# Performance work log

Measured on AMD Instinct MI355X. Metric: run time of the kernel, lower is better.

## Reference

```python
import jax, jax.numpy as jnp
import numpy as np

B, M, T, N = 128, 256, 512, 512

def setup_inputs() -> dict:
    key = jax.random.key(0)
    ks = jax.random.split(key, 6)
    return {
        "hidden_state": jax.random.normal(ks[0], (B, M), jnp.float32),
        "cell_state": jax.random.normal(ks[1], (B, M), jnp.float32),
        "X": jax.random.normal(ks[2], (B, T, N), jnp.float32),
        "We1": jax.random.normal(ks[3], (2 * M, T), jnp.float32) * 0.05,
        "be1": jnp.zeros((T,), jnp.float32),
        "We2": jax.random.normal(ks[4], (T, T), jnp.float32) * 0.05,
        "be2": jnp.zeros((T,), jnp.float32),
        "v": jax.random.normal(ks[5], (T, 1), jnp.float32) * 0.05,
        "bv": jnp.zeros((1,), jnp.float32),
    }

def reference(hidden_state, cell_state, X, We1, be1, We2, be2, v, bv):
    # concat hidden + cell: [B, 2m]; Dense(T) then broadcast over n (K.repeat)
    hc = jnp.concatenate([hidden_state, cell_state], axis=-1)
    hs = (hc @ We1 + be1)[:, None, :]                 # [B, 1, T] (broadcast over n)
    # Permute X -> [B, n, T], Dense(T): contract over T
    ux = jnp.einsum('btn,tk->bnk', X, We2) + be2      # [B, n, T]
    # add + tanh + Dense(1) fused chain
    e = jnp.tanh(hs + ux) @ v + bv                    # [B, n, 1]
    # Permute -> [B, 1, n], softmax over last axis (n)
    attn = jax.nn.softmax(jnp.swapaxes(e, 1, 2), axis=-1)  # [B, 1, n]
    return attn
```

## Files before the change

### kernel.cpp

```cpp
#include <hip/hip_runtime.h>
#include <hip/hip_bf16.h>


typedef _Float16 half8 __attribute__((ext_vector_type(8)));
typedef _Float16 half4 __attribute__((ext_vector_type(4)));
typedef float floatx4 __attribute__((ext_vector_type(4)));

#define GLOAD_LDS16(gp, lp) __builtin_amdgcn_global_load_lds(                  \
    (const __attribute__((address_space(1))) void*)(const void*)(gp),          \
    (__attribute__((address_space(3))) void*)(void*)(lp), 16, 0, 0)

__device__ __forceinline__ float fast_tanh(float x) {
    float cx = fminf(15.0f, fmaxf(-15.0f, x));
    float e = __expf(2.0f * cx);
    return (e - 1.0f) * __fdividef(1.0f, e + 1.0f);
}

__global__ __launch_bounds__(256) void k_prep_a(const float* __restrict__ We2,
                                                _Float16* __restrict__ Af) {
    __shared__ float w2[32][512];
    const int ts = blockIdx.x;
    for (int idx = threadIdx.x; idx < 32 * 512; idx += 256) {
        int tl = idx >> 9, k = idx & 511;
        w2[tl][k] = We2[(ts * 32 + tl) * 512 + k];
    }
    __syncthreads();
    for (int item = threadIdx.x; item < 32 * 64; item += 256) {
        int c = item >> 6, l = item & 63;
        int k  = c * 16 + (l & 15);
        int tl = (l >> 4) * 8;
        half8 h;
#pragma unroll
        for (int j = 0; j < 8; ++j) h[j] = (_Float16)w2[tl + j][k];
        *(half8*)&Af[(((size_t)ts * 32 + c) * 64 + l) * 8] = h;
    }
}

__global__ __launch_bounds__(256) void k_hs(const float* __restrict__ hidden,
                                            const float* __restrict__ cell,
                                            const float* __restrict__ We1,
                                            const float* __restrict__ be1,
                                            const float* __restrict__ be2,
                                            float* __restrict__ g) {
    __shared__ __align__(16) float hcl[8][512];
    __shared__ float red[4][8][64];
    const int b0 = (blockIdx.x >> 3) << 3;
    const int k0 = (blockIdx.x & 7) << 6;
    for (int idx = threadIdx.x; idx < 8 * 512; idx += 256) {
        int bi = idx >> 9, j = idx & 511;
        hcl[bi][j] = (j < 256) ? hidden[(b0 + bi) * 256 + j]
                               : cell[(b0 + bi) * 256 + j - 256];
    }
    __syncthreads();
    const int kl = threadIdx.x & 63;
    const int jc = threadIdx.x >> 6;
    const int k  = k0 + kl;
    float acc[8] = {};
    for (int j = jc * 128; j < jc * 128 + 128; j += 4) {
        float w0 = We1[(j + 0) * 512 + k];
        float w1 = We1[(j + 1) * 512 + k];
        float w2 = We1[(j + 2) * 512 + k];
        float w3 = We1[(j + 3) * 512 + k];
#pragma unroll
        for (int bi = 0; bi < 8; ++bi) {
            float4 h = *(const float4*)&hcl[bi][j];
            acc[bi] += h.x * w0 + h.y * w1 + h.z * w2 + h.w * w3;
        }
    }
#pragma unroll
    for (int bi = 0; bi < 8; ++bi) red[jc][bi][kl] = acc[bi];
    __syncthreads();
    for (int idx = threadIdx.x; idx < 512; idx += 256) {
        int bi = idx >> 6, kk = idx & 63;
        float s = red[0][bi][kk] + red[1][bi][kk] + red[2][bi][kk] + red[3][bi][kk];
        int kg = k0 + kk;
        g[(b0 + bi) * 512 + kg] = s + be1[kg] + be2[kg];
    }
}

__global__ __launch_bounds__(512, 4) void k_main(const float* __restrict__ X,
                                                 const _Float16* __restrict__ Af,
                                                 const float* __restrict__ g,
                                                 const float* __restrict__ vvec,
                                                 float* __restrict__ E) {
    __shared__ __align__(16) _Float16 Ab[2][16384];
    __shared__ __align__(16) _Float16 Xb[2][2048];
    const int b    = blockIdx.x >> 3;
    const int n0   = (blockIdx.x & 7) << 6;
    const int tid  = threadIdx.x;
    const int lane = tid & 63;
    const int wv   = tid >> 6;
    const int l16  = lane & 15;
    const int lhi  = lane >> 4;

    const float* Xg = X + (size_t)b * (512 * 512) + n0;
    const int xn = lane;
    const int xslot = ((xn >> 4) * 64 + (wv >> 1) * 16 + (xn & 15)) * 8 + (wv & 1) * 4;
    const _Float16* AgW = Af + (size_t)wv * 2048 + (size_t)lane * 8;

    float xrA[4], xrB[4];

#pragma unroll
    for (int i = 0; i < 4; ++i)
        GLOAD_LDS16(AgW + i * 512, &Ab[0][wv * 2048 + i * 512 + lane * 8]);
#pragma unroll
    for (int j = 0; j < 4; ++j)
        xrA[j] = Xg[(size_t)(wv * 4 + j) * 512 + xn];
#pragma unroll
    for (int j = 0; j < 4; ++j)
        xrB[j] = Xg[(size_t)(32 + wv * 4 + j) * 512 + xn];
    {
        half4 h;
#pragma unroll
        for (int j = 0; j < 4; ++j) h[j] = (_Float16)xrA[j];
        *(half4*)&Xb[0][xslot] = h;
    }
    asm volatile("s_waitcnt vmcnt(4) lgkmcnt(0)" ::: "memory");
    __builtin_amdgcn_sched_barrier(0);
    __builtin_amdgcn_s_barrier();
    __builtin_amdgcn_sched_barrier(0);

    floatx4 acc[4][4];
#pragma unroll
    for (int a = 0; a < 4; ++a)
#pragma unroll
        for (int c = 0; c < 4; ++c) acc[a][c] = (floatx4){0.f, 0.f, 0.f, 0.f};

#pragma unroll
    for (int ts = 0; ts < 16; ++ts) {
        const int cur = ts & 1;
        const int nxt = cur ^ 1;
        if (ts < 15) {
#pragma unroll
            for (int i = 0; i < 4; ++i)
                GLOAD_LDS16(AgW + (size_t)(ts + 1) * 16384 + i * 512,
                            &Ab[nxt][wv * 2048 + i * 512 + lane * 8]);
        }
        if (ts < 14) {
            if ((ts & 1) == 0) {
#pragma unroll
                for (int j = 0; j < 4; ++j)
                    xrA[j] = Xg[(size_t)((ts + 2) * 32 + wv * 4 + j) * 512 + xn];
            } else {
#pragma unroll
                for (int j = 0; j < 4; ++j)
                    xrB[j] = Xg[(size_t)((ts + 2) * 32 + wv * 4 + j) * 512 + xn];
            }
        }
        if (ts < 15) {
            half4 h;
            if ((ts & 1) == 0) {
#pragma unroll
                for (int j = 0; j < 4; ++j) h[j] = (_Float16)xrB[j];
            } else {
#pragma unroll
                for (int j = 0; j < 4; ++j) h[j] = (_Float16)xrA[j];
            }
            *(half4*)&Xb[nxt][xslot] = h;
        }
        {
            half8 af0 = *(const half8*)&Ab[cur][(wv * 4 + 0) * 512 + lane * 8];
            half8 af1 = *(const half8*)&Ab[cur][(wv * 4 + 1) * 512 + lane * 8];
            half8 af2 = *(const half8*)&Ab[cur][(wv * 4 + 2) * 512 + lane * 8];
            half8 af3 = *(const half8*)&Ab[cur][(wv * 4 + 3) * 512 + lane * 8];
            __builtin_amdgcn_s_setprio(1);
#pragma unroll
            for (int nf = 0; nf < 4; ++nf) {
                half8 bf = *(const half8*)&Xb[cur][(nf * 64 + lane) * 8];
                acc[0][nf] = __builtin_amdgcn_mfma_f32_16x16x32_f16(af0, bf, acc[0][nf], 0, 0, 0);
                acc[1][nf] = __builtin_amdgcn_mfma_f32_16x16x32_f16(af1, bf, acc[1][nf], 0, 0, 0);
                acc[2][nf] = __builtin_amdgcn_mfma_f32_16x16x32_f16(af2, bf, acc[2][nf], 0, 0, 0);
                acc[3][nf] = __builtin_amdgcn_mfma_f32_16x16x32_f16(af3, bf, acc[3][nf], 0, 0, 0);
            }
            __builtin_amdgcn_s_setprio(0);
        }
        if (ts < 15) {
            if (ts < 14) {
                asm volatile("s_waitcnt vmcnt(4) lgkmcnt(0)" ::: "memory");
            } else {
                asm volatile("s_waitcnt vmcnt(0) lgkmcnt(0)" ::: "memory");
            }
            __builtin_amdgcn_sched_barrier(0);
            __builtin_amdgcn_s_barrier();
            __builtin_amdgcn_sched_barrier(0);
        }
    }

    const float* gb = g + b * 512;
    float s[4] = {0.f, 0.f, 0.f, 0.f};
#pragma unroll
    for (int kf = 0; kf < 4; ++kf) {
        const int kb = wv * 64 + kf * 16 + lhi * 4;
        float g0 = gb[kb + 0], g1 = gb[kb + 1], g2 = gb[kb + 2], g3 = gb[kb + 3];
        float v0 = vvec[kb + 0], v1 = vvec[kb + 1], v2 = vvec[kb + 2], v3 = vvec[kb + 3];
#pragma unroll
        for (int nf = 0; nf < 4; ++nf) {
            s[nf] += fast_tanh(acc[kf][nf][0] + g0) * v0;
            s[nf] += fast_tanh(acc[kf][nf][1] + g1) * v1;
            s[nf] += fast_tanh(acc[kf][nf][2] + g2) * v2;
            s[nf] += fast_tanh(acc[kf][nf][3] + g3) * v3;
        }
    }
#pragma unroll
    for (int nf = 0; nf < 4; ++nf) {
        s[nf] += __shfl_xor(s[nf], 16);
        s[nf] += __shfl_xor(s[nf], 32);
    }
    __syncthreads();
    float* ered = (float*)&Ab[0][0];
    if (lane < 16) {
#pragma unroll
        for (int nf = 0; nf < 4; ++nf) ered[wv * 64 + nf * 16 + l16] = s[nf];
    }
    __syncthreads();
    if (tid < 64) {
        float e = 0.f;
#pragma unroll
        for (int w = 0; w < 8; ++w) e += ered[w * 64 + tid];
        E[b * 512 + n0 + tid] = e;
    }
}

__global__ __launch_bounds__(256) void k_softmax(const float* __restrict__ E,
                                                 float* __restrict__ out) {
    __shared__ float rmax[4], rsum[4];
    const int b = blockIdx.x;
    const int tid = threadIdx.x;
    float e0 = E[b * 512 + tid];
    float e1 = E[b * 512 + 256 + tid];
    float m = fmaxf(e0, e1);
    for (int o = 32; o > 0; o >>= 1) m = fmaxf(m, __shfl_xor(m, o));
    if ((tid & 63) == 0) rmax[tid >> 6] = m;
    __syncthreads();
    m = fmaxf(fmaxf(rmax[0], rmax[1]), fmaxf(rmax[2], rmax[3]));
    float p0 = __expf(e0 - m), p1 = __expf(e1 - m);
    float ss = p0 + p1;
    for (int o = 32; o > 0; o >>= 1) ss += __shfl_xor(ss, o);
    if ((tid & 63) == 0) rsum[tid >> 6] = ss;
    __syncthreads();
    ss = rsum[0] + rsum[1] + rsum[2] + rsum[3];
    float inv = __fdividef(1.0f, ss);
    out[b * 512 + tid] = p0 * inv;
    out[b * 512 + 256 + tid] = p1 * inv;
}

extern "C" void kernel_launch(void* const* d_in, const int* in_sizes, int n_in,
                              void* d_out, int out_size, void* d_ws, size_t ws_size,
                              hipStream_t stream) {
    const float* hidden = (const float*)d_in[0];
    const float* cell   = (const float*)d_in[1];
    const float* X      = (const float*)d_in[2];
    const float* We1    = (const float*)d_in[3];
    const float* be1    = (const float*)d_in[4];
    const float* We2    = (const float*)d_in[5];
    const float* be2    = (const float*)d_in[6];
    const float* v      = (const float*)d_in[7];
    float* out = (float*)d_out;

    char* ws = (char*)d_ws;
    _Float16* Af = (_Float16*)ws;
    float* g     = (float*)(ws + 524288);
    float* E     = (float*)(ws + 524288 + 262144);

    k_prep_a<<<16, 256, 0, stream>>>(We2, Af);
    k_hs<<<128, 256, 0, stream>>>(hidden, cell, We1, be1, be2, g);
    k_main<<<1024, 512, 0, stream>>>(X, Af, g, v, E);
    k_softmax<<<128, 256, 0, stream>>>(E, out);
}
```

Measured before the change: 83.27 us.

## Split main kernel across two output-column halves with partial energy buffers

Each k_main block now handles half of the T output columns with 256 threads, so the grid doubles to 2048 blocks and each block's shared A buffer halves. The two blocks write partial energies to separate buffers, and the softmax kernel adds them before normalising. The aim is more, smaller blocks for better occupancy and latency hiding. The cost is that each X tile is now loaded and converted by both sibling blocks, which relies on the L2 cache to absorb the duplicate reads. The change also adds sched_barrier fences to fix instruction ordering in the pipelined loop.

```diff
diff --git a/kernel.cpp b/kernel.cpp
--- a/kernel.cpp
+++ b/kernel.cpp
@@ -3,7 +3,6 @@
 
 
 typedef _Float16 half8 __attribute__((ext_vector_type(8)));
-typedef _Float16 half4 __attribute__((ext_vector_type(4)));
 typedef float floatx4 __attribute__((ext_vector_type(4)));
 
 #define GLOAD_LDS16(gp, lp) __builtin_amdgcn_global_load_lds(                  \
@@ -78,15 +77,17 @@
     }
 }
 
-__global__ __launch_bounds__(512, 4) void k_main(const float* __restrict__ X,
+__global__ __launch_bounds__(256, 4) void k_main(const float* __restrict__ X,
                                                  const _Float16* __restrict__ Af,
                                                  const float* __restrict__ g,
                                                  const float* __restrict__ vvec,
-                                                 float* __restrict__ E) {
-    __shared__ __align__(16) _Float16 Ab[2][16384];
+                                                 float* __restrict__ Ep) {
+    __shared__ __align__(16) _Float16 Ab[2][8192];
     __shared__ __align__(16) _Float16 Xb[2][2048];
-    const int b    = blockIdx.x >> 3;
-    const int n0   = (blockIdx.x & 7) << 6;
+    const int bid  = blockIdx.x;
+    const int ksl  = bid & 1;
+    const int n0   = ((bid >> 1) & 7) << 6;
+    const int b    = bid >> 4;
     const int tid  = threadIdx.x;
     const int lane = tid & 63;
     const int wv   = tid >> 6;
@@ -94,28 +95,29 @@
     const int lhi  = lane >> 4;
 
     const float* Xg = X + (size_t)b * (512 * 512) + n0;
-    const int xn = lane;
-    const int xslot = ((xn >> 4) * 64 + (wv >> 1) * 16 + (xn & 15)) * 8 + (wv & 1) * 4;
-    const _Float16* AgW = Af + (size_t)wv * 2048 + (size_t)lane * 8;
-
-    float xrA[4], xrB[4];
+    const int xn    = tid & 63;
+    const int xo    = wv;
+    const int xslot = ((xn >> 4) * 64 + xo * 16 + (xn & 15)) * 8;
+    const _Float16* AgW = Af + ((size_t)(ksl * 16 + wv * 4)) * 512 + (size_t)lane * 8;
+
+    float xrA[8], xrB[8];
 
 #pragma unroll
     for (int i = 0; i < 4; ++i)
         GLOAD_LDS16(AgW + i * 512, &Ab[0][wv * 2048 + i * 512 + lane * 8]);
 #pragma unroll
-    for (int j = 0; j < 4; ++j)
-        xrA[j] = Xg[(size_t)(wv * 4 + j) * 512 + xn];
-#pragma unroll
-    for (int j = 0; j < 4; ++j)
-        xrB[j] = Xg[(size_t)(32 + wv * 4 + j) * 512 + xn];
+    for (int j = 0; j < 8; ++j)
+        xrA[j] = Xg[(size_t)(xo * 8 + j) * 512 + xn];
+#pragma unroll
+    for (int j = 0; j < 8; ++j)
+        xrB[j] = Xg[(size_t)(32 + xo * 8 + j) * 512 + xn];
     {
-        half4 h;
-#pragma unroll
-        for (int j = 0; j < 4; ++j) h[j] = (_Float16)xrA[j];
-        *(half4*)&Xb[0][xslot] = h;
-    }
-    asm volatile("s_waitcnt vmcnt(4) lgkmcnt(0)" ::: "memory");
+        half8 h;
+#pragma unroll
+        for (int j = 0; j < 8; ++j) h[j] = (_Float16)xrA[j];
+        *(half8*)&Xb[0][xslot] = h;
+    }
+    asm volatile("s_waitcnt vmcnt(8) lgkmcnt(0)" ::: "memory");
     __builtin_amdgcn_sched_barrier(0);
     __builtin_amdgcn_s_barrier();
     __builtin_amdgcn_sched_barrier(0);
@@ -139,25 +141,27 @@
         if (ts < 14) {
             if ((ts & 1) == 0) {
 #pragma unroll
-                for (int j = 0; j < 4; ++j)
-                    xrA[j] = Xg[(size_t)((ts + 2) * 32 + wv * 4 + j) * 512 + xn];
+                for (int j = 0; j < 8; ++j)
+                    xrA[j] = Xg[(size_t)((ts + 2) * 32 + xo * 8 + j) * 512 + xn];
             } else {
 #pragma unroll
-                for (int j = 0; j < 4; ++j)
-                    xrB[j] = Xg[(size_t)((ts + 2) * 32 + wv * 4 + j) * 512 + xn];
-            }
-        }
+                for (int j = 0; j < 8; ++j)
+                    xrB[j] = Xg[(size_t)((ts + 2) * 32 + xo * 8 + j) * 512 + xn];
+            }
+        }
+        __builtin_amdgcn_sched_barrier(0);
         if (ts < 15) {
-            half4 h;
+            half8 h;
             if ((ts & 1) == 0) {
 #pragma unroll
-                for (int j = 0; j < 4; ++j) h[j] = (_Float16)xrB[j];
+                for (int j = 0; j < 8; ++j) h[j] = (_Float16)xrB[j];
             } else {
 #pragma unroll
-                for (int j = 0; j < 4; ++j) h[j] = (_Float16)xrA[j];
-            }
-            *(half4*)&Xb[nxt][xslot] = h;
-        }
+                for (int j = 0; j < 8; ++j) h[j] = (_Float16)xrA[j];
+            }
+            *(half8*)&Xb[nxt][xslot] = h;
+        }
+        __builtin_amdgcn_sched_barrier(0);
         {
             half8 af0 = *(const half8*)&Ab[cur][(wv * 4 + 0) * 512 + lane * 8];
             half8 af1 = *(const half8*)&Ab[cur][(wv * 4 + 1) * 512 + lane * 8];
@@ -174,9 +178,10 @@
             }
             __builtin_amdgcn_s_setprio(0);
         }
+        __builtin_amdgcn_sched_barrier(0);
         if (ts < 15) {
             if (ts < 14) {
-                asm volatile("s_waitcnt vmcnt(4) lgkmcnt(0)" ::: "memory");
+                asm volatile("s_waitcnt vmcnt(8) lgkmcnt(0)" ::: "memory");
             } else {
                 asm volatile("s_waitcnt vmcnt(0) lgkmcnt(0)" ::: "memory");
             }
@@ -190,7 +195,7 @@
     float s[4] = {0.f, 0.f, 0.f, 0.f};
 #pragma unroll
     for (int kf = 0; kf < 4; ++kf) {
-        const int kb = wv * 64 + kf * 16 + lhi * 4;
+        const int kb = ksl * 256 + wv * 64 + kf * 16 + lhi * 4;
         float g0 = gb[kb + 0], g1 = gb[kb + 1], g2 = gb[kb + 2], g3 = gb[kb + 3];
         float v0 = vvec[kb + 0], v1 = vvec[kb + 1], v2 = vvec[kb + 2], v3 = vvec[kb + 3];
 #pragma unroll
@@ -214,20 +219,20 @@
     }
     __syncthreads();
     if (tid < 64) {
-        float e = 0.f;
-#pragma unroll
-        for (int w = 0; w < 8; ++w) e += ered[w * 64 + tid];
-        E[b * 512 + n0 + tid] = e;
-    }
-}
-
-__global__ __launch_bounds__(256) void k_softmax(const float* __restrict__ E,
+        float e = ered[tid] + ered[64 + tid] + ered[128 + tid] + ered[192 + tid];
+        Ep[(size_t)ksl * (128 * 512) + b * 512 + n0 + tid] = e;
+    }
+}
+
+__global__ __launch_bounds__(256) void k_softmax(const float* __restrict__ Ep,
                                                  float* __restrict__ out) {
     __shared__ float rmax[4], rsum[4];
     const int b = blockIdx.x;
     const int tid = threadIdx.x;
-    float e0 = E[b * 512 + tid];
-    float e1 = E[b * 512 + 256 + tid];
+    const float* E0 = Ep;
+    const float* E1 = Ep + 128 * 512;
+    float e0 = E0[b * 512 + tid] + E1[b * 512 + tid];
+    float e1 = E0[b * 512 + 256 + tid] + E1[b * 512 + 256 + tid];
     float m = fmaxf(e0, e1);
     for (int o = 32; o > 0; o >>= 1) m = fmaxf(m, __shfl_xor(m, o));
     if ((tid & 63) == 0) rmax[tid >> 6] = m;
@@ -260,10 +265,10 @@
     char* ws = (char*)d_ws;
     _Float16* Af = (_Float16*)ws;
     float* g     = (float*)(ws + 524288);
-    float* E     = (float*)(ws + 524288 + 262144);
+    float* Ep    = (float*)(ws + 524288 + 262144);
 
     k_prep_a<<<16, 256, 0, stream>>>(We2, Af);
     k_hs<<<128, 256, 0, stream>>>(hidden, cell, We1, be1, be2, g);
-    k_main<<<1024, 512, 0, stream>>>(X, Af, g, v, E);
-    k_softmax<<<128, 256, 0, stream>>>(E, out);
-}
+    k_main<<<2048, 256, 0, stream>>>(X, Af, g, v, Ep);
+    k_softmax<<<128, 256, 0, stream>>>(Ep, out);
+}
```

After: 83.08 us. Within noise of the previous version (-0.2%).
